# Kernel tuning notes

Measured on AMD Instinct MI355X. Metric: run time of the kernel, lower is better.

## Reference

```python
import jax, jax.numpy as jnp
import numpy as np

B, C, H, W = 16, 256, 64, 64
C8 = C // 8


def setup_inputs() -> dict:
    key = jax.random.key(0)
    ks = jax.random.split(key, 8)
    return {
        "x": jax.random.normal(ks[0], (B, C, H, W), dtype=jnp.float32),
        "Wq": jax.random.normal(ks[1], (C8, C), dtype=jnp.float32) * (1.0 / np.sqrt(C)),
        "bq": jax.random.normal(ks[2], (C8,), dtype=jnp.float32) * 0.02,
        "Wk": jax.random.normal(ks[3], (C8, C), dtype=jnp.float32) * (1.0 / np.sqrt(C)),
        "bk": jax.random.normal(ks[4], (C8,), dtype=jnp.float32) * 0.02,
        "Wv": jax.random.normal(ks[5], (C, C), dtype=jnp.float32) * (1.0 / np.sqrt(C)),
        "bv": jax.random.normal(ks[6], (C,), dtype=jnp.float32) * 0.02,
        "gamma": jax.random.normal(ks[7], (1,), dtype=jnp.float32),
    }


def reference(x, Wq, bq, Wk, bk, Wv, bv, gamma):
    b, c, h, w = x.shape
    n = h * w
    xf = x.reshape(b, c, n)  # [B, C, N]
    # 1x1 convs == per-pixel linear projections
    q = jnp.einsum('oc,bcn->bon', Wq, xf) + bq[None, :, None]  # [B, C/8, N]
    k = jnp.einsum('oc,bcn->bon', Wk, xf) + bk[None, :, None]  # [B, C/8, N]
    v = jnp.einsum('oc,bcn->bon', Wv, xf) + bv[None, :, None]  # [B, C, N]
    # energy[b,i,j] = sum_c q[b,c,i] * k[b,c,j]
    energy = jnp.einsum('bci,bcj->bij', q, k)  # [B, N, N]
    att = jax.nn.softmax(energy, axis=-1)
    # out[b,c,i] = sum_j v[b,c,j] * att[b,i,j]  (bmm(V, att^T))
    out = jnp.einsum('bcj,bij->bci', v, att)
    return (gamma[0] * out + xf).reshape(b, c, h, w)
```

## Files before the change

### kernel.cpp

```cpp
#include <hip/hip_runtime.h>
#include <stdint.h>

#define BATCH 16
#define CH    256
#define CQ    32
#define NPIX  4096
#define WROWS 320

typedef float f32x4 __attribute__((ext_vector_type(4)));
typedef short s16x8 __attribute__((ext_vector_type(8)));

__device__ __forceinline__ ushort f2bf(float f){
  union { float f; uint32_t u; } a; a.f = f;
  uint32_t r = a.u + 0x7FFFu + ((a.u >> 16) & 1u);
  return (ushort)(r >> 16);
}
__device__ __forceinline__ float bf2f(ushort h){
  union { float f; uint32_t u; } a; a.u = ((uint32_t)h) << 16; return a.f;
}
__device__ __forceinline__ void gload16(const void* g, void* l){
  __builtin_amdgcn_global_load_lds(
      (const __attribute__((address_space(1))) uint32_t*)g,
      (__attribute__((address_space(3))) uint32_t*)l, 16, 0, 0);
}

__global__ __launch_bounds__(256) void prep_w(
    const float* __restrict__ Wq, const float* __restrict__ Wk,
    const float* __restrict__ Wv,
    ushort* __restrict__ whi, ushort* __restrict__ wlo)
{
  int idx = blockIdx.x*256 + threadIdx.x;
  int r = idx >> 8;
  float f = (r < 32) ? Wq[idx] : (r < 64) ? Wk[idx - 32*CH] : Wv[idx - 64*CH];
  ushort h = f2bf(f);
  whi[idx] = h;
  wlo[idx] = f2bf(f - bf2f(h));
}

__global__ __launch_bounds__(256,2) void proj_mfma(
    const float* __restrict__ x,
    const ushort* __restrict__ whi, const ushort* __restrict__ wlo,
    const float* __restrict__ bq, const float* __restrict__ bk,
    const float* __restrict__ bv,
    ushort* __restrict__ qhi, ushort* __restrict__ qlo,
    ushort* __restrict__ khi, ushort* __restrict__ klo,
    ushort* __restrict__ vt)
{
  __shared__ __align__(16) float xT[64*256];
  const int b  = blockIdx.y;
  const int n0 = blockIdx.x * 64;
  const int t  = threadIdx.x;
  const int wu = __builtin_amdgcn_readfirstlane(t >> 6);
  const int l  = t & 63;
  const int g  = l >> 4, li = l & 15, lsw = l & 7;

  {
    const float* xb = x + ((size_t)b*CH)*NPIX + n0 + l;
    #pragma unroll
    for (int cq = 0; cq < 16; ++cq) {
      int c4 = wu*64 + cq*4;
      f32x4 v;
      v[0] = xb[(size_t)(c4+0)*NPIX];
      v[1] = xb[(size_t)(c4+1)*NPIX];
      v[2] = xb[(size_t)(c4+2)*NPIX];
      v[3] = xb[(size_t)(c4+3)*NPIX];
      int phys = (c4 >> 2) ^ lsw;
      *(f32x4*)&xT[l*256 + phys*4] = v;
    }
  }
  __syncthreads();

  f32x4 acc[5][4];
  #pragma unroll
  for (int ct=0;ct<5;++ct)
    #pragma unroll
    for (int nt=0;nt<4;++nt) acc[ct][nt] = (f32x4){0.f,0.f,0.f,0.f};

  #pragma unroll 1
  for (int ks = 0; ks < 8; ++ks) {
    s16x8 wh[5], wl[5];
    #pragma unroll
    for (int ct = 0; ct < 5; ++ct) {
      size_t off = (size_t)(wu*80 + ct*16 + li)*CH + ks*32 + g*8;
      wh[ct] = *(const s16x8*)(whi + off);
      wl[ct] = *(const s16x8*)(wlo + off);
    }
    s16x8 xh[4], xl[4];
    #pragma unroll
    for (int nt = 0; nt < 4; ++nt) {
      int row = nt*16 + li;
      int ch0 = ks*8 + 2*g;
      f32x4 a0 = *(const f32x4*)&xT[row*256 + ((ch0    ) ^ (li&7))*4];
      f32x4 a1 = *(const f32x4*)&xT[row*256 + ((ch0 + 1) ^ (li&7))*4];
      float fv[8] = {a0[0],a0[1],a0[2],a0[3],a1[0],a1[1],a1[2],a1[3]};
      union { ushort u[8]; s16x8 v; } ph, pl;
      #pragma unroll
      for (int e=0;e<8;++e){
        ushort h = f2bf(fv[e]); ph.u[e] = h; pl.u[e] = f2bf(fv[e] - bf2f(h));
      }
      xh[nt] = ph.v; xl[nt] = pl.v;
    }
    #pragma unroll
    for (int ct=0;ct<5;++ct)
      #pragma unroll
      for (int nt=0;nt<4;++nt){
        acc[ct][nt] = __builtin_amdgcn_mfma_f32_16x16x32_bf16(wh[ct], xh[nt], acc[ct][nt], 0,0,0);
        acc[ct][nt] = __builtin_amdgcn_mfma_f32_16x16x32_bf16(wh[ct], xl[nt], acc[ct][nt], 0,0,0);
        acc[ct][nt] = __builtin_amdgcn_mfma_f32_16x16x32_bf16(wl[ct], xh[nt], acc[ct][nt], 0,0,0);
      }
  }

  const int rsub = g*4;
  #pragma unroll
  for (int ct = 0; ct < 5; ++ct) {
    const int cog = wu*80 + ct*16;
    if (cog < 64) {
      const float*  bias = (cog < 32) ? bq  : bk;
      ushort*       dhi  = (cog < 32) ? qhi : khi;
      ushort*       dlo  = (cog < 32) ? qlo : klo;
      const int cb = (cog & 31) + rsub;
      float4 bi = *(const float4*)(bias + cb);
      #pragma unroll
      for (int nt = 0; nt < 4; ++nt) {
        int n = n0 + nt*16 + li;
        union { ushort u[4]; uint2 v; } ph, pl;
        #pragma unroll
        for (int r = 0; r < 4; ++r) {
          float val = acc[ct][nt][r] + ((const float*)&bi)[r];
          ushort h = f2bf(val);
          ph.u[r] = h; pl.u[r] = f2bf(val - bf2f(h));
        }
        size_t base = ((size_t)b*NPIX + n)*CQ + cb;
        *(uint2*)(dhi + base) = ph.v;
        *(uint2*)(dlo + base) = pl.v;
      }
    } else {
      const int vr = cog - 64 + rsub;
      float4 bi = *(const float4*)(bv + vr);
      #pragma unroll
      for (int nt = 0; nt < 4; ++nt) {
        int n = n0 + nt*16 + li;
        #pragma unroll
        for (int r = 0; r < 4; ++r)
          vt[((size_t)b*CH + vr + r)*NPIX + n] =
              f2bf(acc[ct][nt][r] + ((const float*)&bi)[r]);
      }
    }
  }
}

__global__ __launch_bounds__(256,2) void attn_kernel(
    const ushort* __restrict__ qhi, const ushort* __restrict__ qlo,
    const ushort* __restrict__ khi, const ushort* __restrict__ klo,
    const ushort* __restrict__ vt,  const float* __restrict__ x,
    const float* __restrict__ gamma, float* __restrict__ out)
{
  __shared__ __align__(16) ushort vtile[2][CH*64];
  __shared__ __align__(16) ushort ptile[4][32*64];

  const int flat = blockIdx.x + (int)gridDim.x * blockIdx.y;
  const int nf   = (flat & 7)*64 + (flat >> 3);
  const int b    = nf >> 5;
  const int i0   = (nf & 31) << 7;

  const int t   = threadIdx.x;
  const int wu  = __builtin_amdgcn_readfirstlane(t >> 6);
  const int l   = t & 63, lhi = l >> 4, llo = l & 15;

  const int crow = l >> 3;
  const int jsw  = ((l & 7) ^ crow) * 8;
  const uint32_t vbase = (uint32_t)((b*CH + wu*64 + crow)*NPIX) + (uint32_t)jsw;

  s16x8 qh[2], qlf[2];
  #pragma unroll
  for (int rt=0; rt<2; ++rt){
    size_t off = ((size_t)b*NPIX + i0 + wu*32 + rt*16 + llo)*CQ + lhi*8;
    qh[rt]  = *(const s16x8*)(qhi + off);
    qlf[rt] = *(const s16x8*)(qlo + off);
  }

  f32x4 acc[16][2];
  #pragma unroll
  for (int ct=0;ct<16;++ct){
    acc[ct][0] = (f32x4){0.f,0.f,0.f,0.f};
    acc[ct][1] = (f32x4){0.f,0.f,0.f,0.f};
  }
  float m0=-1e30f, m1=-1e30f, ls0=0.f, ls1=0.f;

  ushort* pt = ptile[wu];
  const ushort* kbh = khi + (size_t)b*NPIX*CQ;
  const ushort* kbl = klo + (size_t)b*NPIX*CQ;
  const int kofs_lane = llo*CQ + lhi*8;

  #pragma unroll
  for (int k=0;k<8;++k)
    gload16(vt + vbase + (uint32_t)(k*8*NPIX), &vtile[0][(wu*64 + k*8)*64]);
  __syncthreads();

  #pragma unroll 1
  for (int tt=0; tt<64; ++tt){
    const int cur = tt & 1;

    s16x8 kh[4], kl2[4];
    #pragma unroll
    for (int jt=0;jt<4;++jt){
      int ko = tt*64*CQ + jt*16*CQ + kofs_lane;
      kh[jt]  = *(const s16x8*)(kbh + ko);
      kl2[jt] = *(const s16x8*)(kbl + ko);
    }
    __builtin_amdgcn_sched_barrier(0);
    if (tt < 63){
      const uint32_t src = vbase + (uint32_t)((tt+1)*64);
      #pragma unroll
      for (int k=0;k<8;++k)
        gload16(vt + src + (uint32_t)(k*8*NPIX),
                &vtile[cur^1][(wu*64 + k*8)*64]);
    }

    f32x4 st[2][4];
    #pragma unroll
    for (int rt=0;rt<2;++rt)
      #pragma unroll
      for (int jt=0;jt<4;++jt) st[rt][jt] = (f32x4){0.f,0.f,0.f,0.f};
    __builtin_amdgcn_s_setprio(1);
    #pragma unroll
    for (int jt=0;jt<4;++jt){
      #pragma unroll
      for (int rt=0;rt<2;++rt){
        st[rt][jt] = __builtin_amdgcn_mfma_f32_16x16x32_bf16(kh[jt],  qh[rt],  st[rt][jt], 0,0,0);
        st[rt][jt] = __builtin_amdgcn_mfma_f32_16x16x32_bf16(kl2[jt], qh[rt],  st[rt][jt], 0,0,0);
        st[rt][jt] = __builtin_amdgcn_mfma_f32_16x16x32_bf16(kh[jt],  qlf[rt], st[rt][jt], 0,0,0);
      }
    }
    __builtin_amdgcn_s_setprio(0);

    float mt0 = st[0][0][0], mt1 = st[1][0][0];
    #pragma unroll
    for (int jt=0;jt<4;++jt)
      #pragma unroll
      for (int r=0;r<4;++r){
        mt0 = fmaxf(mt0, st[0][jt][r]);
        mt1 = fmaxf(mt1, st[1][jt][r]);
      }
    mt0 = fmaxf(mt0, __shfl_xor(mt0, 16)); mt0 = fmaxf(mt0, __shfl_xor(mt0, 32));
    mt1 = fmaxf(mt1, __shfl_xor(mt1, 16)); mt1 = fmaxf(mt1, __shfl_xor(mt1, 32));
    int keep = (mt0 <= m0 + 8.f) && (mt1 <= m1 + 8.f);
    if (!__all(keep)){
      float n0m = fmaxf(m0, mt0), n1m = fmaxf(m1, mt1);
      float f0 = __expf(m0 - n0m), f1 = __expf(m1 - n1m);
      m0 = n0m; m1 = n1m; ls0 *= f0; ls1 *= f1;
      #pragma unroll
      for (int ct=0;ct<16;++ct){ acc[ct][0] *= f0; acc[ct][1] *= f1; }
    }
    #pragma unroll
    for (int rt=0;rt<2;++rt){
      float mr = rt ? m1 : m0;
      float lacc = 0.f;
      int il = rt*16 + llo;
      #pragma unroll
      for (int jt=0;jt<4;++jt){
        union { ushort u[4]; uint2 v; } pk;
        #pragma unroll
        for (int r=0;r<4;++r){
          float p = __expf(st[rt][jt][r] - mr);
          lacc += p;
          pk.u[r] = f2bf(p);
        }
        int jcb = jt*2 + (lhi>>1);
        int sub = lhi & 1;
        *(uint2*)&pt[il*64 + ((jcb ^ (il&7))<<3) + sub*4] = pk.v;
      }
      if (rt) ls1 += lacc; else ls0 += lacc;
    }
    s16x8 pf[2][2];
    #pragma unroll
    for (int it=0; it<2; ++it){
      int il = it*16 + llo;
      #pragma unroll
      for (int jh=0; jh<2; ++jh)
        pf[it][jh] = *(const s16x8*)&pt[il*64 + (((jh*4+lhi) ^ (il&7))<<3)];
    }
    __builtin_amdgcn_s_setprio(1);
    #pragma unroll
    for (int ct=0; ct<16; ++ct){
      int c = ct*16 + llo;
      #pragma unroll
      for (int jh=0; jh<2; ++jh){
        s16x8 vf = *(const s16x8*)&vtile[cur][c*64 + (((jh*4+lhi) ^ (c&7))<<3)];
        acc[ct][0] = __builtin_amdgcn_mfma_f32_16x16x32_bf16(vf, pf[0][jh], acc[ct][0], 0,0,0);
        acc[ct][1] = __builtin_amdgcn_mfma_f32_16x16x32_bf16(vf, pf[1][jh], acc[ct][1], 0,0,0);
      }
    }
    __builtin_amdgcn_s_setprio(0);
    __syncthreads();
  }

  ls0 += __shfl_xor(ls0,16); ls0 += __shfl_xor(ls0,32);
  ls1 += __shfl_xor(ls1,16); ls1 += __shfl_xor(ls1,32);
  float rinv0 = 1.f/ls0, rinv1 = 1.f/ls1;
  float gmv = gamma[0];
  #pragma unroll
  for (int ct=0; ct<16; ++ct){
    #pragma unroll
    for (int it=0; it<2; ++it){
      float ri = it ? rinv1 : rinv0;
      #pragma unroll
      for (int r=0;r<4;++r){
        int c  = ct*16 + lhi*4 + r;
        int ii = i0 + wu*32 + it*16 + llo;
        size_t o = ((size_t)b*CH + c)*NPIX + ii;
        out[o] = gmv * acc[ct][it][r] * ri + x[o];
      }
    }
  }
}

extern "C" void kernel_launch(void* const* d_in, const int* in_sizes, int n_in,
                              void* d_out, int out_size, void* d_ws, size_t ws_size,
                              hipStream_t stream)
{
  (void)in_sizes; (void)n_in; (void)out_size; (void)ws_size;
  const float* x     = (const float*)d_in[0];
  const float* Wq    = (const float*)d_in[1];
  const float* bq    = (const float*)d_in[2];
  const float* Wk    = (const float*)d_in[3];
  const float* bk    = (const float*)d_in[4];
  const float* Wv    = (const float*)d_in[5];
  const float* bv    = (const float*)d_in[6];
  const float* gamma = (const float*)d_in[7];
  float* out = (float*)d_out;

  ushort* ws = (ushort*)d_ws;
  const size_t qk_elems = (size_t)BATCH*NPIX*CQ;
  ushort* qhi = ws;
  ushort* qlo = qhi + qk_elems;
  ushort* khi = qlo + qk_elems;
  ushort* klo = khi + qk_elems;
  ushort* vt  = klo + qk_elems;
  ushort* whi = vt  + (size_t)BATCH*CH*NPIX;
  ushort* wlo = whi + (size_t)WROWS*CH;

  prep_w<<<dim3(WROWS), dim3(256), 0, stream>>>(Wq, Wk, Wv, whi, wlo);
  dim3 gp(64, BATCH);
  proj_mfma<<<gp, dim3(256), 0, stream>>>(x, whi, wlo, bq, bk, bv,
                                          qhi, qlo, khi, klo, vt);
  dim3 ga(32, BATCH);
  attn_kernel<<<ga, dim3(256), 0, stream>>>(qhi, qlo, khi, klo, vt, x, gamma, out);
}
```

Baseline: 365.8 us.

## Halve attention query and key tiles to raise occupancy and block count

Shrinks each attention block from 128 to 64 query rows (16 per wave) and the key tile from 64 to 32 columns. This halves the accumulator registers and LDS per block, allowing three blocks per CU and doubling the grid to 1024 blocks. In exchange, V tiles are reloaded twice as often in total, since each V tile is now reused by half as many query rows. There are also twice as many loop iterations and barriers.

```diff
diff --git a/kernel.cpp b/kernel.cpp
--- a/kernel.cpp
+++ b/kernel.cpp
@@ -149,43 +149,39 @@
   }
 }
 
-__global__ __launch_bounds__(256,2) void attn_kernel(
+__global__ __launch_bounds__(256,3) void attn_kernel(
     const ushort* __restrict__ qhi, const ushort* __restrict__ qlo,
     const ushort* __restrict__ khi, const ushort* __restrict__ klo,
     const ushort* __restrict__ vt,  const float* __restrict__ x,
     const float* __restrict__ gamma, float* __restrict__ out)
 {
-  __shared__ __align__(16) ushort vtile[2][CH*64];
-  __shared__ __align__(16) ushort ptile[4][32*64];
+  __shared__ __align__(16) ushort vtile[2][CH*32];
+  __shared__ __align__(16) ushort ptile[4][16*32];
 
   const int flat = blockIdx.x + (int)gridDim.x * blockIdx.y;
-  const int nf   = (flat & 7)*64 + (flat >> 3);
-  const int b    = nf >> 5;
-  const int i0   = (nf & 31) << 7;
+  const int nf   = (flat & 7)*128 + (flat >> 3);
+  const int b    = nf >> 6;
+  const int i0   = (nf & 63) << 6;
 
   const int t   = threadIdx.x;
   const int wu  = __builtin_amdgcn_readfirstlane(t >> 6);
   const int l   = t & 63, lhi = l >> 4, llo = l & 15;
 
-  const int crow = l >> 3;
-  const int jsw  = ((l & 7) ^ crow) * 8;
+  const int crow = l >> 2;
+  const int jsw  = ((l & 3) ^ (crow & 3)) * 8;
   const uint32_t vbase = (uint32_t)((b*CH + wu*64 + crow)*NPIX) + (uint32_t)jsw;
 
-  s16x8 qh[2], qlf[2];
-  #pragma unroll
-  for (int rt=0; rt<2; ++rt){
-    size_t off = ((size_t)b*NPIX + i0 + wu*32 + rt*16 + llo)*CQ + lhi*8;
-    qh[rt]  = *(const s16x8*)(qhi + off);
-    qlf[rt] = *(const s16x8*)(qlo + off);
-  }
-
-  f32x4 acc[16][2];
-  #pragma unroll
-  for (int ct=0;ct<16;++ct){
-    acc[ct][0] = (f32x4){0.f,0.f,0.f,0.f};
-    acc[ct][1] = (f32x4){0.f,0.f,0.f,0.f};
-  }
-  float m0=-1e30f, m1=-1e30f, ls0=0.f, ls1=0.f;
+  s16x8 qh, qlf;
+  {
+    size_t off = ((size_t)b*NPIX + i0 + wu*16 + llo)*CQ + lhi*8;
+    qh  = *(const s16x8*)(qhi + off);
+    qlf = *(const s16x8*)(qlo + off);
+  }
+
+  f32x4 acc[16];
+  #pragma unroll
+  for (int ct=0;ct<16;++ct) acc[ct] = (f32x4){0.f,0.f,0.f,0.f};
+  float m = -1e30f, ls = 0.f;
 
   ushort* pt = ptile[wu];
   const ushort* kbh = khi + (size_t)b*NPIX*CQ;
@@ -193,124 +189,96 @@
   const int kofs_lane = llo*CQ + lhi*8;
 
   #pragma unroll
-  for (int k=0;k<8;++k)
-    gload16(vt + vbase + (uint32_t)(k*8*NPIX), &vtile[0][(wu*64 + k*8)*64]);
+  for (int k=0;k<4;++k)
+    gload16(vt + vbase + (uint32_t)(k*16*NPIX), &vtile[0][(wu*64 + k*16)*32]);
   __syncthreads();
 
   #pragma unroll 1
-  for (int tt=0; tt<64; ++tt){
+  for (int tt=0; tt<128; ++tt){
     const int cur = tt & 1;
 
-    s16x8 kh[4], kl2[4];
-    #pragma unroll
-    for (int jt=0;jt<4;++jt){
-      int ko = tt*64*CQ + jt*16*CQ + kofs_lane;
+    s16x8 kh[2], kl2[2];
+    #pragma unroll
+    for (int jt=0;jt<2;++jt){
+      int ko = (tt*32 + jt*16)*CQ + kofs_lane;
       kh[jt]  = *(const s16x8*)(kbh + ko);
       kl2[jt] = *(const s16x8*)(kbl + ko);
     }
     __builtin_amdgcn_sched_barrier(0);
-    if (tt < 63){
-      const uint32_t src = vbase + (uint32_t)((tt+1)*64);
-      #pragma unroll
-      for (int k=0;k<8;++k)
-        gload16(vt + src + (uint32_t)(k*8*NPIX),
-                &vtile[cur^1][(wu*64 + k*8)*64]);
-    }
-
-    f32x4 st[2][4];
-    #pragma unroll
-    for (int rt=0;rt<2;++rt)
-      #pragma unroll
-      for (int jt=0;jt<4;++jt) st[rt][jt] = (f32x4){0.f,0.f,0.f,0.f};
+    if (tt < 127){
+      const uint32_t src = vbase + (uint32_t)((tt+1)*32);
+      #pragma unroll
+      for (int k=0;k<4;++k)
+        gload16(vt + src + (uint32_t)(k*16*NPIX),
+                &vtile[cur^1][(wu*64 + k*16)*32]);
+    }
+
+    f32x4 st[2];
+    st[0] = (f32x4){0.f,0.f,0.f,0.f};
+    st[1] = (f32x4){0.f,0.f,0.f,0.f};
     __builtin_amdgcn_s_setprio(1);
     #pragma unroll
-    for (int jt=0;jt<4;++jt){
-      #pragma unroll
-      for (int rt=0;rt<2;++rt){
-        st[rt][jt] = __builtin_amdgcn_mfma_f32_16x16x32_bf16(kh[jt],  qh[rt],  st[rt][jt], 0,0,0);
-        st[rt][jt] = __builtin_amdgcn_mfma_f32_16x16x32_bf16(kl2[jt], qh[rt],  st[rt][jt], 0,0,0);
-        st[rt][jt] = __builtin_amdgcn_mfma_f32_16x16x32_bf16(kh[jt],  qlf[rt], st[rt][jt], 0,0,0);
-      }
+    for (int jt=0;jt<2;++jt){
+      st[jt] = __builtin_amdgcn_mfma_f32_16x16x32_bf16(kh[jt],  qh,  st[jt], 0,0,0);
+      st[jt] = __builtin_amdgcn_mfma_f32_16x16x32_bf16(kl2[jt], qh,  st[jt], 0,0,0);
+      st[jt] = __builtin_amdgcn_mfma_f32_16x16x32_bf16(kh[jt],  qlf, st[jt], 0,0,0);
     }
     __builtin_amdgcn_s_setprio(0);
 
-    float mt0 = st[0][0][0], mt1 = st[1][0][0];
-    #pragma unroll
-    for (int jt=0;jt<4;++jt)
-      #pragma unroll
-      for (int r=0;r<4;++r){
-        mt0 = fmaxf(mt0, st[0][jt][r]);
-        mt1 = fmaxf(mt1, st[1][jt][r]);
-      }
-    mt0 = fmaxf(mt0, __shfl_xor(mt0, 16)); mt0 = fmaxf(mt0, __shfl_xor(mt0, 32));
-    mt1 = fmaxf(mt1, __shfl_xor(mt1, 16)); mt1 = fmaxf(mt1, __shfl_xor(mt1, 32));
-    int keep = (mt0 <= m0 + 8.f) && (mt1 <= m1 + 8.f);
+    float mt = st[0][0];
+    #pragma unroll
+    for (int jt=0;jt<2;++jt)
+      #pragma unroll
+      for (int r=0;r<4;++r) mt = fmaxf(mt, st[jt][r]);
+    mt = fmaxf(mt, __shfl_xor(mt, 16)); mt = fmaxf(mt, __shfl_xor(mt, 32));
+    int keep = (mt <= m + 8.f);
     if (!__all(keep)){
-      float n0m = fmaxf(m0, mt0), n1m = fmaxf(m1, mt1);
-      float f0 = __expf(m0 - n0m), f1 = __expf(m1 - n1m);
-      m0 = n0m; m1 = n1m; ls0 *= f0; ls1 *= f1;
-      #pragma unroll
-      for (int ct=0;ct<16;++ct){ acc[ct][0] *= f0; acc[ct][1] *= f1; }
-    }
-    #pragma unroll
-    for (int rt=0;rt<2;++rt){
-      float mr = rt ? m1 : m0;
+      float nm = fmaxf(m, mt);
+      float f = __expf(m - nm);
+      m = nm; ls *= f;
+      #pragma unroll
+      for (int ct=0;ct<16;++ct) acc[ct] *= f;
+    }
+    {
       float lacc = 0.f;
-      int il = rt*16 + llo;
-      #pragma unroll
-      for (int jt=0;jt<4;++jt){
+      #pragma unroll
+      for (int jt=0;jt<2;++jt){
         union { ushort u[4]; uint2 v; } pk;
         #pragma unroll
         for (int r=0;r<4;++r){
-          float p = __expf(st[rt][jt][r] - mr);
+          float p = __expf(st[jt][r] - m);
           lacc += p;
           pk.u[r] = f2bf(p);
         }
         int jcb = jt*2 + (lhi>>1);
         int sub = lhi & 1;
-        *(uint2*)&pt[il*64 + ((jcb ^ (il&7))<<3) + sub*4] = pk.v;
-      }
-      if (rt) ls1 += lacc; else ls0 += lacc;
-    }
-    s16x8 pf[2][2];
-    #pragma unroll
-    for (int it=0; it<2; ++it){
-      int il = it*16 + llo;
-      #pragma unroll
-      for (int jh=0; jh<2; ++jh)
-        pf[it][jh] = *(const s16x8*)&pt[il*64 + (((jh*4+lhi) ^ (il&7))<<3)];
-    }
+        *(uint2*)&pt[llo*32 + ((jcb ^ (llo&3))<<3) + sub*4] = pk.v;
+      }
+      ls += lacc;
+    }
+    s16x8 pf = *(const s16x8*)&pt[llo*32 + ((lhi ^ (llo&3))<<3)];
     __builtin_amdgcn_s_setprio(1);
     #pragma unroll
     for (int ct=0; ct<16; ++ct){
       int c = ct*16 + llo;
-      #pragma unroll
-      for (int jh=0; jh<2; ++jh){
-        s16x8 vf = *(const s16x8*)&vtile[cur][c*64 + (((jh*4+lhi) ^ (c&7))<<3)];
-        acc[ct][0] = __builtin_amdgcn_mfma_f32_16x16x32_bf16(vf, pf[0][jh], acc[ct][0], 0,0,0);
-        acc[ct][1] = __builtin_amdgcn_mfma_f32_16x16x32_bf16(vf, pf[1][jh], acc[ct][1], 0,0,0);
-      }
+      s16x8 vf = *(const s16x8*)&vtile[cur][c*32 + ((lhi ^ (c&3))<<3)];
+      acc[ct] = __builtin_amdgcn_mfma_f32_16x16x32_bf16(vf, pf, acc[ct], 0,0,0);
     }
     __builtin_amdgcn_s_setprio(0);
     __syncthreads();
   }
 
-  ls0 += __shfl_xor(ls0,16); ls0 += __shfl_xor(ls0,32);
-  ls1 += __shfl_xor(ls1,16); ls1 += __shfl_xor(ls1,32);
-  float rinv0 = 1.f/ls0, rinv1 = 1.f/ls1;
+  ls += __shfl_xor(ls,16); ls += __shfl_xor(ls,32);
+  float rinv = 1.f/ls;
   float gmv = gamma[0];
   #pragma unroll
   for (int ct=0; ct<16; ++ct){
     #pragma unroll
-    for (int it=0; it<2; ++it){
-      float ri = it ? rinv1 : rinv0;
-      #pragma unroll
-      for (int r=0;r<4;++r){
-        int c  = ct*16 + lhi*4 + r;
-        int ii = i0 + wu*32 + it*16 + llo;
-        size_t o = ((size_t)b*CH + c)*NPIX + ii;
-        out[o] = gmv * acc[ct][it][r] * ri + x[o];
-      }
+    for (int r=0;r<4;++r){
+      int c  = ct*16 + lhi*4 + r;
+      int ii = i0 + wu*16 + llo;
+      size_t o = ((size_t)b*CH + c)*NPIX + ii;
+      out[o] = gmv * acc[ct][r] * rinv + x[o];
     }
   }
 }
@@ -344,6 +312,6 @@
   dim3 gp(64, BATCH);
   proj_mfma<<<gp, dim3(256), 0, stream>>>(x, whi, wlo, bq, bk, bv,
                                           qhi, qlo, khi, klo, vt);
-  dim3 ga(32, BATCH);
+  dim3 ga(64, BATCH);
   attn_kernel<<<ga, dim3(256), 0, stream>>>(qhi, qlo, khi, klo, vt, x, gamma, out);
 }
```

Result: slower. 428.5 us (+17.1%).
